# Kernel optimization log

Hardware: AMD Instinct MI355X
Metric: run time of the kernel (lower is better)

Reference implementation:

```python
import jax, jax.numpy as jnp
import numpy as np

B, S, D = 256, 1024, 32   # batch, seq_len, raw feature dim
H, L = 128, 2             # hidden_dim, num_layers
IN = D + 2                # GRU input: features + mask + time-delta


def setup_inputs() -> dict:
    key = jax.random.key(0)
    ks = jax.random.split(key, 16)
    x = jax.random.normal(ks[0], (B, S, D), jnp.float32)
    nan_mask = jax.random.bernoulli(ks[1], 0.3, (B, S))
    x = jnp.where(nan_mask[:, :, None], jnp.nan, x)  # missing timesteps are all-NaN
    # strictly increasing timestamps shared across batch
    t = jnp.cumsum(jax.random.uniform(ks[2], (S,), jnp.float32, 0.1, 1.0))

    def init(k, shape):
        s = 1.0 / np.sqrt(H)
        return jax.random.uniform(k, shape, jnp.float32, -s, s)

    params = {}
    in_dims = [IN, H]
    for l in range(L):
        params[f"Wih{l}"] = init(ks[3 + 4 * l], (3 * H, in_dims[l]))
        params[f"Whh{l}"] = init(ks[4 + 4 * l], (3 * H, H))
        params[f"bih{l}"] = init(ks[5 + 4 * l], (3 * H,))
        params[f"bhh{l}"] = init(ks[6 + 4 * l], (3 * H,))
    return {"t": t, "x": x, **params}


def _impute(t, x):
    # mask[b,i] = 1 if timestep i of sample b is missing (any NaN feature)
    mask = jnp.isnan(x).any(-1)                      # [B,S] bool
    # prev[b,i] = last observed index strictly before i, or -1 (parallel cummax)
    idx = jnp.where(~mask, jnp.arange(S)[None, :], -1)
    cmax = jax.lax.cummax(idx, axis=1)
    prev = jnp.concatenate([jnp.full((B, 1), -1), cmax[:, :-1]], axis=1)  # [B,S]
    prev_c = jnp.clip(prev, 0, S - 1)
    x_clean = jnp.nan_to_num(x)
    x_prev = jnp.take_along_axis(x_clean, prev_c[:, :, None], axis=1)
    # masked: forward-fill from last observation (zeros if none); unmasked: keep x
    imputed = jnp.where(mask[:, :, None],
                        jnp.where((prev >= 0)[:, :, None], x_prev, 0.0),
                        x_clean)
    # time delta: t[i]-t[prev] when a previous observation exists, else raw t delta
    t_deltas = jnp.concatenate([jnp.zeros((1,), t.dtype), t[1:] - t[:-1]])
    t_exp = jnp.where(prev >= 0, t[None, :] - t[prev_c], t_deltas[None, :])  # [B,S]
    return jnp.concatenate([imputed,
                            mask.astype(jnp.float32)[:, :, None],
                            t_exp[:, :, None]], axis=-1)  # [B,S,D+2]


def _gru_layer(xseq, Wih, Whh, bih, bhh):
    # precompute input projections for all timesteps (one big GEMM)
    gx = jnp.einsum('bsd,gd->bsg', xseq, Wih) + bih  # [B,S,3H], gate order r,z,n

    def step(h, g):
        gh = h @ Whh.T + bhh
        r = jax.nn.sigmoid(g[:, :H] + gh[:, :H])
        z = jax.nn.sigmoid(g[:, H:2 * H] + gh[:, H:2 * H])
        n = jnp.tanh(g[:, 2 * H:] + r * gh[:, 2 * H:])
        h = (1.0 - z) * n + z * h
        return h, h

    h0 = jnp.zeros((xseq.shape[0], H), xseq.dtype)
    _, hs = jax.lax.scan(step, h0, gx.transpose(1, 0, 2))
    return hs.transpose(1, 0, 2)  # [B,S,H]


def reference(t, x, Wih0, Whh0, bih0, bhh0, Wih1, Whh1, bih1, bhh1):
    inp = _impute(t, x)
    h = _gru_layer(inp, Wih0, Whh0, bih0, bhh0)
    h = _gru_layer(h, Wih1, Whh1, bih1, bhh1)
    return h[:, -1, :]  # [B,H]
```

## Files before the change

kernel.cpp:

```cpp
#include <hip/hip_runtime.h>
#include <hip/hip_bf16.h>


#define BB 256
#define SS 1024
#define DD 32
#define HH 128
#define NT 768

typedef _Float16 f16;
typedef __attribute__((ext_vector_type(2))) _Float16 h2;

__device__ inline h2 as_h2(int x) { union { int i; h2 h; } u; u.i = x; return u.h; }

__device__ inline float dot2(h2 a, h2 b, float c) {
    return __builtin_amdgcn_fdot2(a, b, c, false);
}

__device__ inline float frcp(float x) { return __builtin_amdgcn_rcpf(x); }
__device__ inline float fast_sigm(float x) { return frcp(1.0f + __expf(-x)); }
__device__ inline float fast_tanh(float x) {
    x = fminf(15.0f, fmaxf(-15.0f, x));
    float e = __expf(-2.0f * x);
    return (1.0f - e) * frcp(1.0f + e);
}

struct ImpState { float xprev, tprev; bool hasprev; };

__device__ inline void impute_store(int i, float xv, int l, ImpState& st,
                                    f16* hxf, const float* tb) {
    bool nanp = (l < 32) && (xv != xv);
    unsigned long long bal = __ballot(nanp);
    bool mask = bal != 0ull;
    if (l < 32) {
        float imp = mask ? st.xprev : xv;
        hxf[l] = (f16)imp;
        if (!mask) st.xprev = xv;
    }
    float tcur = tb[i];
    float tdel = (i == 0) ? 0.0f : (tcur - tb[i - 1]);
    float texp = st.hasprev ? (tcur - st.tprev) : tdel;
    if (l == 32) hxf[32] = (f16)(mask ? 1.0f : 0.0f);
    if (l == 33) hxf[33] = (f16)texp;
    if (!mask) { st.hasprev = true; st.tprev = tcur; }
}

__global__ __launch_bounds__(NT, 3) void gru_fused(
    const float* __restrict__ t_in, const float* __restrict__ x_in,
    const float* __restrict__ Wih0, const float* __restrict__ Whh0,
    const float* __restrict__ bih0, const float* __restrict__ bhh0,
    const float* __restrict__ Wih1, const float* __restrict__ Whh1,
    const float* __restrict__ bih1, const float* __restrict__ bhh1,
    float* __restrict__ out)
{
    __shared__ float tb[SS];
    __shared__ int stDW[152];
    __shared__ float pA[NT], pC[NT], pD[NT], pE[NT];

    const int tid = threadIdx.x;
    const int b = blockIdx.x;
    const int group = tid >= 384;
    const int row = tid - 384 * group;
    const int lane = tid & 63;

    h2 wih0[9], whh0[32], wih1[32], whh1[32];
    {
        const float* p = Wih0 + row * 34;
        const int lim = 8 + group;
        #pragma unroll
        for (int k = 0; k < 9; k++) {
            int e = 16 * group + 2 * k;
            f16 lo = (k < lim) ? (f16)p[e]     : (f16)0.0f;
            f16 hi = (k < lim) ? (f16)p[e + 1] : (f16)0.0f;
            h2 v = {lo, hi}; wih0[k] = v;
        }
        p = Whh0 + row * HH + 64 * group;
        #pragma unroll
        for (int k = 0; k < 32; k++) { h2 v = {(f16)p[2*k], (f16)p[2*k+1]}; whh0[k] = v; }
        p = Wih1 + row * HH + 64 * group;
        #pragma unroll
        for (int k = 0; k < 32; k++) { h2 v = {(f16)p[2*k], (f16)p[2*k+1]}; wih1[k] = v; }
        p = Whh1 + row * HH + 64 * group;
        #pragma unroll
        for (int k = 0; k < 32; k++) { h2 v = {(f16)p[2*k], (f16)p[2*k+1]}; whh1[k] = v; }
    }

    const bool isU = (tid >= 512);
    const bool isU0 = (tid >= 512 && tid < 640);
    const int j = isU0 ? (tid - 512) : (tid - 640);
    float ubi[3], ubh[3]; float hr = 0.0f;
    if (isU) {
        const float* bi = isU0 ? bih0 : bih1;
        const float* bh = isU0 ? bhh0 : bhh1;
        #pragma unroll
        for (int q = 0; q < 3; q++) { ubi[q] = bi[j + 128*q]; ubh[q] = bh[j + 128*q]; }
    }

    const int idxA = (lane < 32) ? (32 * group + lane)
                                 : (64 + 32 * group + (lane - 32));
    const int idxB = 128 + 8 * group + ((lane < 9) ? lane : 0);

    for (int i2 = tid; i2 < SS; i2 += NT) tb[i2] = t_in[i2];
    if (tid < 152) stDW[tid] = 0;

    f16* h0f = (f16*)&stDW[0];
    f16* h1f = (f16*)&stDW[64];
    f16* hxf = (f16*)&stDW[128];

    const float* xrow = x_in + (size_t)b * SS * DD + tid;
    ImpState st; st.xprev = 0.0f; st.tprev = 0.0f; st.hasprev = false;

    __syncthreads();
    if (tid < 64) {
        float xv0 = (tid < 32) ? xrow[0] : 0.0f;
        impute_store(0, xv0, tid, st, hxf, tb);
    }
    __syncthreads();

    for (int i = 0; i <= SS; ++i) {
        const bool doL0 = (i < SS), doL1 = (i > 0), doImp = (i + 1 < SS);

        int vA = stDW[idxA];
        int vB = stDW[idxB];

        float xv_n = 0.0f;
        if (tid < 32 && doImp) xv_n = xrow[(size_t)(i + 1) * DD];

        int h0u[32], h1u[32], hxu[9];
        #pragma unroll
        for (int k = 0; k < 32; k++) h0u[k] = __builtin_amdgcn_readlane(vA, k);
        #pragma unroll
        for (int k = 0; k < 32; k++) h1u[k] = __builtin_amdgcn_readlane(vA, 32 + k);
        #pragma unroll
        for (int k = 0; k < 9; k++)  hxu[k] = __builtin_amdgcn_readlane(vB, k);

        float aP = 0.0f;
        #pragma unroll
        for (int k = 0; k < 9; k++) aP = dot2(as_h2(hxu[k]), wih0[k], aP);
        float cC[4] = {0,0,0,0}, dC[4] = {0,0,0,0}, eC[4] = {0,0,0,0};
        #pragma unroll
        for (int k = 0; k < 32; k++) {
            h2 hh = as_h2(h0u[k]);
            cC[k & 3] = dot2(hh, whh0[k], cC[k & 3]);
            dC[k & 3] = dot2(hh, wih1[k], dC[k & 3]);
        }
        #pragma unroll
        for (int k = 0; k < 32; k++) {
            h2 hh = as_h2(h1u[k]);
            eC[k & 3] = dot2(hh, whh1[k], eC[k & 3]);
        }
        pA[tid] = aP;
        pC[tid] = (cC[0] + cC[1]) + (cC[2] + cC[3]);
        pD[tid] = (dC[0] + dC[1]) + (dC[2] + dC[3]);
        pE[tid] = (eC[0] + eC[1]) + (eC[2] + eC[3]);
        __syncthreads();

        if (isU) {
            bool act = isU0 ? doL0 : doL1;
            if (act) {
                float rx, rh, zx, zh, nx, nh;
                if (isU0) {
                    rx = pA[j]       + pA[384 + j];       rh = pC[j]       + pC[384 + j];
                    zx = pA[j + 128] + pA[384 + j + 128]; zh = pC[j + 128] + pC[384 + j + 128];
                    nx = pA[j + 256] + pA[384 + j + 256]; nh = pC[j + 256] + pC[384 + j + 256];
                } else {
                    rx = pD[j]       + pD[384 + j];       rh = pE[j]       + pE[384 + j];
                    zx = pD[j + 128] + pD[384 + j + 128]; zh = pE[j + 128] + pE[384 + j + 128];
                    nx = pD[j + 256] + pD[384 + j + 256]; nh = pE[j + 256] + pE[384 + j + 256];
                }
                float r = fast_sigm(ubi[0] + ubh[0] + rx + rh);
                float z = fast_sigm(ubi[1] + ubh[1] + zx + zh);
                float n = fast_tanh(ubi[2] + nx + r * (ubh[2] + nh));
                hr = (1.0f - z) * n + z * hr;
                (isU0 ? h0f : h1f)[j] = (f16)hr;
            }
        } else if (tid < 64 && doImp) {
            impute_store(i + 1, xv_n, tid, st, hxf, tb);
        }
        __syncthreads();
    }

    if (tid >= 640) out[(size_t)b * HH + (tid - 640)] = hr;
}

extern "C" void kernel_launch(void* const* d_in, const int* in_sizes, int n_in,
                              void* d_out, int out_size, void* d_ws, size_t ws_size,
                              hipStream_t stream) {
    gru_fused<<<dim3(BB), dim3(NT), 0, stream>>>(
        (const float*)d_in[0], (const float*)d_in[1],
        (const float*)d_in[2], (const float*)d_in[3],
        (const float*)d_in[4], (const float*)d_in[5],
        (const float*)d_in[6], (const float*)d_in[7],
        (const float*)d_in[8], (const float*)d_in[9],
        (float*)d_out);
}
```

Before: 1.570 ms.

## Shrink block to 512 threads and drop split-K partial sums in fused GRU

```diff
diff --git a/kernel.cpp b/kernel.cpp
--- a/kernel.cpp
+++ b/kernel.cpp
@@ -6,7 +6,7 @@
 #define SS 1024
 #define DD 32
 #define HH 128
-#define NT 768
+#define NT 512
 
 typedef _Float16 f16;
 typedef __attribute__((ext_vector_type(2))) _Float16 h2;
@@ -45,7 +45,7 @@
     if (!mask) { st.hasprev = true; st.tprev = tcur; }
 }
 
-__global__ __launch_bounds__(NT, 3) void gru_fused(
+__global__ __launch_bounds__(NT, 2) void gru_fused(
     const float* __restrict__ t_in, const float* __restrict__ x_in,
     const float* __restrict__ Wih0, const float* __restrict__ Whh0,
     const float* __restrict__ bih0, const float* __restrict__ bhh0,
@@ -54,57 +54,55 @@
     float* __restrict__ out)
 {
     __shared__ float tb[SS];
-    __shared__ int stDW[152];
-    __shared__ float pA[NT], pC[NT], pD[NT], pE[NT];
+    __shared__ int stDW[145];
+    __shared__ float pGX0[384], pGH0[384], pGX1[384], pGH1[384];
 
     const int tid = threadIdx.x;
+    const int lane = tid & 63;
     const int b = blockIdx.x;
-    const int group = tid >= 384;
-    const int row = tid - 384 * group;
-    const int lane = tid & 63;
+    const bool isDot = (tid < 384);
 
-    h2 wih0[9], whh0[32], wih1[32], whh1[32];
-    {
-        const float* p = Wih0 + row * 34;
-        const int lim = 8 + group;
+    h2 w[192];
+    if (isDot) {
+        const float* pa = Whh0 + tid * HH;
+        const float* pb = Wih1 + tid * HH;
+        const float* pc = Wih0 + tid * 34;
         #pragma unroll
-        for (int k = 0; k < 9; k++) {
-            int e = 16 * group + 2 * k;
-            f16 lo = (k < lim) ? (f16)p[e]     : (f16)0.0f;
-            f16 hi = (k < lim) ? (f16)p[e + 1] : (f16)0.0f;
-            h2 v = {lo, hi}; wih0[k] = v;
-        }
-        p = Whh0 + row * HH + 64 * group;
+        for (int k = 0; k < 64; k++) { h2 v = {(f16)pa[2*k], (f16)pa[2*k+1]}; w[k] = v; }
         #pragma unroll
-        for (int k = 0; k < 32; k++) { h2 v = {(f16)p[2*k], (f16)p[2*k+1]}; whh0[k] = v; }
-        p = Wih1 + row * HH + 64 * group;
+        for (int k = 0; k < 64; k++) { h2 v = {(f16)pb[2*k], (f16)pb[2*k+1]}; w[64+k] = v; }
         #pragma unroll
-        for (int k = 0; k < 32; k++) { h2 v = {(f16)p[2*k], (f16)p[2*k+1]}; wih1[k] = v; }
-        p = Whh1 + row * HH + 64 * group;
+        for (int k = 0; k < 17; k++) { h2 v = {(f16)pc[2*k], (f16)pc[2*k+1]}; w[128+k] = v; }
         #pragma unroll
-        for (int k = 0; k < 32; k++) { h2 v = {(f16)p[2*k], (f16)p[2*k+1]}; whh1[k] = v; }
+        for (int k = 145; k < 192; k++) { h2 v = {(f16)0.0f, (f16)0.0f}; w[k] = v; }
+    } else {
+        const int gl = tid - 384;
+        const float* p0 = Whh1 + (size_t)gl * HH;
+        const float* p1 = Whh1 + (size_t)(gl + 128) * HH;
+        const float* p2 = Whh1 + (size_t)(gl + 256) * HH;
+        #pragma unroll
+        for (int k = 0; k < 64; k++) { h2 v = {(f16)p0[2*k], (f16)p0[2*k+1]}; w[k] = v; }
+        #pragma unroll
+        for (int k = 0; k < 64; k++) { h2 v = {(f16)p1[2*k], (f16)p1[2*k+1]}; w[64+k] = v; }
+        #pragma unroll
+        for (int k = 0; k < 64; k++) { h2 v = {(f16)p2[2*k], (f16)p2[2*k+1]}; w[128+k] = v; }
     }
 
-    const bool isU = (tid >= 512);
-    const bool isU0 = (tid >= 512 && tid < 640);
-    const int j = isU0 ? (tid - 512) : (tid - 640);
-    float ubi[3], ubh[3]; float hr = 0.0f;
-    if (isU) {
-        const float* bi = isU0 ? bih0 : bih1;
-        const float* bh = isU0 ? bhh0 : bhh1;
-        #pragma unroll
-        for (int q = 0; q < 3; q++) { ubi[q] = bi[j + 128*q]; ubh[q] = bh[j + 128*q]; }
+    float hra = 0.0f, hrb = 0.0f;
+    float bra = 0, bza = 0, bina = 0, bhna = 0, brb = 0, bzb = 0, binb = 0, bhnb = 0;
+    if (!isDot) {
+        const bool u0 = (tid < 448);
+        const float* bi = u0 ? bih0 : bih1;
+        const float* bh = u0 ? bhh0 : bhh1;
+        const int ua = 2 * lane, ub = ua + 1;
+        bra = bi[ua] + bh[ua];       bza = bi[ua+128] + bh[ua+128];
+        bina = bi[ua+256];           bhna = bh[ua+256];
+        brb = bi[ub] + bh[ub];       bzb = bi[ub+128] + bh[ub+128];
+        binb = bi[ub+256];           bhnb = bh[ub+256];
     }
 
-    const int idxA = (lane < 32) ? (32 * group + lane)
-                                 : (64 + 32 * group + (lane - 32));
-    const int idxB = 128 + 8 * group + ((lane < 9) ? lane : 0);
-
     for (int i2 = tid; i2 < SS; i2 += NT) tb[i2] = t_in[i2];
-    if (tid < 152) stDW[tid] = 0;
-
-    f16* h0f = (f16*)&stDW[0];
-    f16* h1f = (f16*)&stDW[64];
+    if (tid < 128) stDW[tid] = 0;
     f16* hxf = (f16*)&stDW[128];
 
     const float* xrow = x_in + (size_t)b * SS * DD + tid;
@@ -117,62 +115,62 @@
     }
     __syncthreads();
 
+    const int idxA = isDot ? lane : (64 + lane);
+    const int idxB = 128 + ((lane < 17) ? lane : 0);
+
     for (int i = 0; i <= SS; ++i) {
         const bool doL0 = (i < SS), doL1 = (i > 0), doImp = (i + 1 < SS);
 
         int vA = stDW[idxA];
-        int vB = stDW[idxB];
 
         float xv_n = 0.0f;
         if (tid < 32 && doImp) xv_n = xrow[(size_t)(i + 1) * DD];
 
-        int h0u[32], h1u[32], hxu[9];
-        #pragma unroll
-        for (int k = 0; k < 32; k++) h0u[k] = __builtin_amdgcn_readlane(vA, k);
-        #pragma unroll
-        for (int k = 0; k < 32; k++) h1u[k] = __builtin_amdgcn_readlane(vA, 32 + k);
-        #pragma unroll
-        for (int k = 0; k < 9; k++)  hxu[k] = __builtin_amdgcn_readlane(vB, k);
-
-        float aP = 0.0f;
-        #pragma unroll
-        for (int k = 0; k < 9; k++) aP = dot2(as_h2(hxu[k]), wih0[k], aP);
-        float cC[4] = {0,0,0,0}, dC[4] = {0,0,0,0}, eC[4] = {0,0,0,0};
-        #pragma unroll
-        for (int k = 0; k < 32; k++) {
-            h2 hh = as_h2(h0u[k]);
-            cC[k & 3] = dot2(hh, whh0[k], cC[k & 3]);
-            dC[k & 3] = dot2(hh, wih1[k], dC[k & 3]);
+        if (isDot) {
+            int vB = stDW[idxB];
+            float aGH0 = 0.0f, aGX1 = 0.0f, aGX0 = 0.0f;
+            #pragma unroll
+            for (int k = 0; k < 64; k++) {
+                h2 s = as_h2(__builtin_amdgcn_readlane(vA, k));
+                aGH0 = dot2(s, w[k],      aGH0);
+                aGX1 = dot2(s, w[64 + k], aGX1);
+            }
+            #pragma unroll
+            for (int k = 0; k < 17; k++) {
+                h2 s = as_h2(__builtin_amdgcn_readlane(vB, k));
+                aGX0 = dot2(s, w[128 + k], aGX0);
+            }
+            pGH0[tid] = aGH0; pGX1[tid] = aGX1; pGX0[tid] = aGX0;
+        } else {
+            const int gl = tid - 384;
+            float a0 = 0.0f, a1 = 0.0f, a2 = 0.0f;
+            #pragma unroll
+            for (int k = 0; k < 64; k++) {
+                h2 s = as_h2(__builtin_amdgcn_readlane(vA, k));
+                a0 = dot2(s, w[k],       a0);
+                a1 = dot2(s, w[64 + k],  a1);
+                a2 = dot2(s, w[128 + k], a2);
+            }
+            pGH1[gl] = a0; pGH1[gl + 128] = a1; pGH1[gl + 256] = a2;
         }
-        #pragma unroll
-        for (int k = 0; k < 32; k++) {
-            h2 hh = as_h2(h1u[k]);
-            eC[k & 3] = dot2(hh, whh1[k], eC[k & 3]);
-        }
-        pA[tid] = aP;
-        pC[tid] = (cC[0] + cC[1]) + (cC[2] + cC[3]);
-        pD[tid] = (dC[0] + dC[1]) + (dC[2] + dC[3]);
-        pE[tid] = (eC[0] + eC[1]) + (eC[2] + eC[3]);
         __syncthreads();
 
-        if (isU) {
-            bool act = isU0 ? doL0 : doL1;
-            if (act) {
-                float rx, rh, zx, zh, nx, nh;
-                if (isU0) {
-                    rx = pA[j]       + pA[384 + j];       rh = pC[j]       + pC[384 + j];
-                    zx = pA[j + 128] + pA[384 + j + 128]; zh = pC[j + 128] + pC[384 + j + 128];
-                    nx = pA[j + 256] + pA[384 + j + 256]; nh = pC[j + 256] + pC[384 + j + 256];
-                } else {
-                    rx = pD[j]       + pD[384 + j];       rh = pE[j]       + pE[384 + j];
-                    zx = pD[j + 128] + pD[384 + j + 128]; zh = pE[j + 128] + pE[384 + j + 128];
-                    nx = pD[j + 256] + pD[384 + j + 256]; nh = pE[j + 256] + pE[384 + j + 256];
-                }
-                float r = fast_sigm(ubi[0] + ubh[0] + rx + rh);
-                float z = fast_sigm(ubi[1] + ubh[1] + zx + zh);
-                float n = fast_tanh(ubi[2] + nx + r * (ubh[2] + nh));
-                hr = (1.0f - z) * n + z * hr;
-                (isU0 ? h0f : h1f)[j] = (f16)hr;
+        if (!isDot) {
+            const bool u0 = (tid < 448);
+            if (u0 ? doL0 : doL1) {
+                const float* gx = u0 ? pGX0 : pGX1;
+                const float* gh = u0 ? pGH0 : pGH1;
+                const int ua = 2 * lane, ub = ua + 1;
+                float r0 = fast_sigm(bra + gx[ua] + gh[ua]);
+                float z0 = fast_sigm(bza + gx[ua+128] + gh[ua+128]);
+                float n0 = fast_tanh(bina + gx[ua+256] + r0 * (bhna + gh[ua+256]));
+                hra = (1.0f - z0) * n0 + z0 * hra;
+                float r1 = fast_sigm(brb + gx[ub] + gh[ub]);
+                float z1 = fast_sigm(bzb + gx[ub+128] + gh[ub+128]);
+                float n1 = fast_tanh(binb + gx[ub+256] + r1 * (bhnb + gh[ub+256]));
+                hrb = (1.0f - z1) * n1 + z1 * hrb;
+                h2 hv = {(f16)hra, (f16)hrb};
+                ((h2*)stDW)[(u0 ? 0 : 64) + lane] = hv;
             }
         } else if (tid < 64 && doImp) {
             impute_store(i + 1, xv_n, tid, st, hxf, tb);
@@ -180,7 +178,10 @@
         __syncthreads();
     }
 
-    if (tid >= 640) out[(size_t)b * HH + (tid - 640)] = hr;
+    if (tid >= 448) {
+        float2 o = make_float2(hra, hrb);
+        *(float2*)&out[(size_t)b * HH + 2 * lane] = o;
+    }
 }
 
 extern "C" void kernel_launch(void* const* d_in, const int* in_sizes, int n_in,
```

Result: no change. 1.548 ms (-1.4%).
